# Kernel tuning notes

Hardware: AMD Instinct MI355X
Metric: run time of the kernel (lower is better)

## Reference

```python
import jax, jax.numpy as jnp
import numpy as np

N = 128       # n_channels
B = 131072    # batch
C = np.float32(np.sqrt(0.5))  # 50/50 beamsplitter amplitude (c = s = sqrt(0.5))


def setup_inputs() -> dict:
    key = jax.random.key(0)
    k1, k2, k3, k4 = jax.random.split(key, 4)
    M = N * (N - 1) // 2
    return {
        "x_real": jax.random.normal(k1, (B, N), jnp.float32),
        "x_imag": jax.random.normal(k2, (B, N), jnp.float32),
        "mzi_phases": jax.random.normal(k3, (M * 2,), jnp.float32) * 0.1,
        "output_phases": jax.random.normal(k4, (N,), jnp.float32) * 0.1,
    }


def _construct_unitary(mzi_phases, output_phases):
    n = output_phases.shape[0]
    m = n * (n - 1) // 2
    # pair ordering matches the torch double loop: i ascending, then j > i (row-major triu)
    i_np, j_np = np.triu_indices(n, 1)
    i_idx = jnp.asarray(i_np, jnp.int32)
    j_idx = jnp.asarray(j_np, jnp.int32)
    ph = mzi_phases.reshape(m, 2)
    theta, phi = ph[:, 0], ph[:, 1]

    def step(U, xs):
        th, ph_, i, j = xs
        e_phi = jax.lax.complex(jnp.cos(ph_), jnp.sin(ph_))
        e_th = jax.lax.complex(jnp.cos(th), jnp.sin(th))
        ri = U[i]
        rj = U[j]
        # T_ij @ U touches only rows i and j (O(N) Givens row update)
        new_i = C * ri + (C * e_phi) * rj
        new_j = (C * e_th) * ri - (C * e_th * e_phi) * rj
        U = U.at[i].set(new_i).at[j].set(new_j)
        return U, None

    def chunk_body(U, xs_chunk):
        U, _ = jax.lax.scan(step, U, xs_chunk)
        return U, None

    # chunk the M sequential updates: M = (n-1) * (n//2) for even n;
    # checkpointing chunks keeps reverse-mode memory O(sqrt-ish) instead of O(M * N^2)
    n_chunks = n - 1
    cs = n // 2
    xs = (theta.reshape(n_chunks, cs), phi.reshape(n_chunks, cs),
          i_idx.reshape(n_chunks, cs), j_idx.reshape(n_chunks, cs))
    U0 = jnp.eye(n, dtype=jnp.complex64)
    U, _ = jax.lax.scan(jax.checkpoint(chunk_body), U0, xs)
    # output phase screen D @ U
    d = jax.lax.complex(jnp.cos(output_phases), jnp.sin(output_phases))
    return d[:, None] * U


def reference(x_real, x_imag, mzi_phases, output_phases):
    U = _construct_unitary(mzi_phases, output_phases)           # [N, N] complex64
    x = jax.lax.complex(x_real, x_imag)                          # [B, N] complex64
    # matmul(U, x.unsqueeze(-1)).squeeze(-1) == x @ U^T
    out = jnp.einsum('nm,bm->bn', U, x)                          # [B, N] complex64
    # ComplexDropout is identity in eval mode
    return out
```

## Files before the change

### kernel.cpp

```cpp
#include <hip/hip_runtime.h>
#include <hip/hip_bf16.h>

#define NDIM 128
#define BDIM 131072
#define NMZI 8128
#define NCHUNK 8
#define CSTEP (NMZI / NCHUNK)
#define NJG 8
#define NCOL 32
#define NLOC 16
static constexpr float CC = 0.70710678118654752440f;

typedef __attribute__((ext_vector_type(8))) short bf16x8;
typedef __attribute__((ext_vector_type(4))) float f32x4;

__device__ __align__(16) float2         g_V[NCHUNK * NDIM * NDIM];
__device__ __align__(16) float2         g_W[4 * NDIM * NDIM];
__device__ __align__(16) float2         g_Y[2 * NDIM * NDIM];
__device__ __align__(16) unsigned short g_TB[32 * NDIM * 8];
__device__ __align__(16) unsigned short g_Ur[16 * NDIM * 8];
__device__ __align__(16) unsigned short g_Ui[16 * NDIM * 8];

__device__ inline unsigned short f2bf(float f) {
    union { __hip_bfloat16 h; unsigned short u; } cv;
    cv.h = __float2bfloat16(f);
    return cv.u;
}

__global__ __launch_bounds__(256) void build_scan(const float* __restrict__ mzi) {
    __shared__ float2 Usm[NDIM][NCOL];
    __shared__ float4 phs[CSTEP];
    __shared__ float4 comp[NJG][NCOL];
    const int tid   = threadIdx.x;
    const int c     = tid & 31;
    const int g     = tid >> 5;
    const int col0  = blockIdx.x * NCOL;
    const int chunk = blockIdx.y;
    const int s0 = chunk * CSTEP, s1 = s0 + CSTEP;

    for (int k = g; k < NDIM; k += NJG)
        Usm[k][c] = make_float2((k == col0 + c) ? 1.f : 0.f, 0.f);
    const float2* mzp = (const float2*)mzi;
    for (int t = tid; t < CSTEP; t += 256) {
        const float2 mz = mzp[s0 + t];
        float sp, cp, st, ct;
        sincosf(mz.y, &sp, &cp);
        sincosf(mz.x, &st, &ct);
        phs[t] = make_float4(cp, sp, CC * ct, CC * st);
    }
    __syncthreads();

    int i = 0, base = 0;
    while (base + (NDIM - 1 - i) <= s0) { base += NDIM - 1 - i; ++i; }

    int s = s0;
    while (s < s1) {
        const int cnt  = NDIM - 1 - i;
        const int jA   = i + 1 + (s - base);
        const int L    = min(s1, base + cnt) - s;
        const int nloc = (L + NJG - 1) >> 3;
        const int myBeg = g * nloc;
        const int myN   = max(0, min(nloc, L - myBeg));
        const int pbase = s - s0;

        const float2 r0 = Usm[i][c];

        float2 treg[NLOC];
        float2 qth[NLOC];
        float  A = 1.f;
        float2 Bc = make_float2(0.f, 0.f);
        #pragma unroll
        for (int kk = 0; kk < NLOC; ++kk) {
            if (kk < myN) {
                const int off = myBeg + kk;
                const float4 q  = phs[pbase + off];
                const float2 rj = Usm[jA + off][c];
                const float tr = fmaf(q.x, rj.x, -q.y * rj.y);
                const float ti = fmaf(q.x, rj.y,  q.y * rj.x);
                treg[kk] = make_float2(tr, ti);
                qth[kk]  = make_float2(q.z, q.w);
                Bc.x = CC * (Bc.x + tr);
                Bc.y = CC * (Bc.y + ti);
                A *= CC;
            }
        }
        comp[g][c] = make_float4(A, Bc.x, Bc.y, 0.f);
        __syncthreads();

        float2 r = r0;
        for (int h = 0; h < g; ++h) {
            const float4 cm = comp[h][c];
            r.x = fmaf(cm.x, r.x, cm.y);
            r.y = fmaf(cm.x, r.y, cm.z);
        }

        #pragma unroll
        for (int kk = 0; kk < NLOC; ++kk) {
            if (kk < myN) {
                const float2 t = treg[kk];
                const float2 q = qth[kk];
                const float dr = r.x - t.x, di = r.y - t.y;
                const float njx = fmaf(q.x, dr, -q.y * di);
                const float njy = fmaf(q.x, di,  q.y * dr);
                Usm[jA + myBeg + kk][c] = make_float2(njx, njy);
                r.x = CC * (r.x + t.x);
                r.y = CC * (r.y + t.y);
            }
        }
        if (myN > 0 && (myBeg + myN == L))
            Usm[i][c] = r;
        __syncthreads();

        s += L;
        if (s == base + cnt) { base += cnt; ++i; }
    }

    float2* Vp = g_V + chunk * NDIM * NDIM;
    for (int k = g; k < NDIM; k += NJG)
        Vp[k * NDIM + col0 + c] = Usm[k][c];
}

__global__ __launch_bounds__(128) void compose(int level) {
    const int p = blockIdx.y, n = blockIdx.x, m = threadIdx.x;
    const float2* A; const float2* B; float2* Cout;
    if (level == 0) {
        A = g_V + (2 * p + 1) * NDIM * NDIM;
        B = g_V + (2 * p) * NDIM * NDIM;
        Cout = g_W + p * NDIM * NDIM;
    } else {
        A = g_W + (2 * p + 1) * NDIM * NDIM;
        B = g_W + (2 * p) * NDIM * NDIM;
        Cout = g_Y + p * NDIM * NDIM;
    }
    __shared__ float2 arow[NDIM];
    arow[m] = A[n * NDIM + m];
    __syncthreads();
    float cr = 0.f, ci = 0.f;
    #pragma unroll 8
    for (int k = 0; k < NDIM; ++k) {
        const float2 b = B[k * NDIM + m];
        const float2 a = arow[k];
        cr = fmaf(a.x, b.x, fmaf(-a.y, b.y, cr));
        ci = fmaf(a.x, b.y, fmaf( a.y, b.x, ci));
    }
    Cout[n * NDIM + m] = make_float2(cr, ci);
}

__global__ __launch_bounds__(128) void compose_final(const float* __restrict__ oph) {
    const int n = blockIdx.x, m = threadIdx.x;
    const float2* A = g_Y + NDIM * NDIM;
    const float2* B = g_Y;
    __shared__ float2 arow[NDIM];
    arow[m] = A[n * NDIM + m];
    __syncthreads();
    float cr = 0.f, ci = 0.f;
    #pragma unroll 8
    for (int k = 0; k < NDIM; ++k) {
        const float2 b = B[k * NDIM + m];
        const float2 a = arow[k];
        cr = fmaf(a.x, b.x, fmaf(-a.y, b.y, cr));
        ci = fmaf(a.x, b.y, fmaf( a.y, b.x, ci));
    }
    float ds, dc;
    sincosf(oph[n], &ds, &dc);
    const float vr = fmaf(cr, dc, -ci * ds);
    const float vi = fmaf(cr, ds,  ci * dc);
    const int kg = m >> 3, e = m & 7;
    g_TB[(kg * NDIM + n) * 8 + e]            = f2bf(vr);
    g_TB[((16 + kg) * NDIM + n) * 8 + e]     = f2bf(-vi);
    g_Ur[(kg * NDIM + n) * 8 + e] = f2bf(vr);
    g_Ui[(kg * NDIM + n) * 8 + e] = f2bf(vi);
}

__global__ __launch_bounds__(256, 2) void cmatmul0(const float* __restrict__ xr,
                                                   const float* __restrict__ xi,
                                                   float* __restrict__ out) {
    __shared__ bf16x8 smT[32 * NDIM];
    const int tid  = threadIdx.x;
    const int lane = tid & 63;
    const int w    = tid >> 6;
    const int r15  = lane & 15;
    const int kg4  = lane >> 4;
    const int rbase = blockIdx.x * 256 + w * 16 + r15;

    float4 bufA[16], bufB[16];
    {
        const float* xrp = xr + (size_t)rbase * NDIM;
        const float* xip = xi + (size_t)rbase * NDIM;
        #pragma unroll
        for (int kc = 0; kc < 4; ++kc) {
            const int k0 = kc * 32 + kg4 * 8;
            bufA[kc * 2]     = *(const float4*)(xrp + k0);
            bufA[kc * 2 + 1] = *(const float4*)(xrp + k0 + 4);
            bufA[8 + kc * 2]     = *(const float4*)(xip + k0);
            bufA[8 + kc * 2 + 1] = *(const float4*)(xip + k0 + 4);
        }
    }
    const bf16x8* gT = (const bf16x8*)g_TB;
    for (int t = tid; t < 32 * NDIM; t += 256) smT[t] = gT[t];
    __syncthreads();

    #pragma unroll
    for (int t = 0; t < 4; ++t) {
        float4* cur = (t & 1) ? bufB : bufA;
        float4* nxt = (t & 1) ? bufA : bufB;
        if (t < 3) {
            const int rn = rbase + (t + 1) * 64;
            const float* xrp = xr + (size_t)rn * NDIM;
            const float* xip = xi + (size_t)rn * NDIM;
            #pragma unroll
            for (int kc = 0; kc < 4; ++kc) {
                const int k0 = kc * 32 + kg4 * 8;
                nxt[kc * 2]     = *(const float4*)(xrp + k0);
                nxt[kc * 2 + 1] = *(const float4*)(xrp + k0 + 4);
                nxt[8 + kc * 2]     = *(const float4*)(xip + k0);
                nxt[8 + kc * 2 + 1] = *(const float4*)(xip + k0 + 4);
            }
        }
        bf16x8 fx[8];
        #pragma unroll
        for (int kc2 = 0; kc2 < 8; ++kc2) {
            const float4 lo = cur[kc2 * 2];
            const float4 hi = cur[kc2 * 2 + 1];
            bf16x8 v;
            v[0] = (short)f2bf(lo.x); v[1] = (short)f2bf(lo.y);
            v[2] = (short)f2bf(lo.z); v[3] = (short)f2bf(lo.w);
            v[4] = (short)f2bf(hi.x); v[5] = (short)f2bf(hi.y);
            v[6] = (short)f2bf(hi.z); v[7] = (short)f2bf(hi.w);
            fx[kc2] = v;
        }
        const size_t orow = (size_t)(rbase + t * 64) * NDIM;
        #pragma unroll
        for (int nt = 0; nt < 8; ++nt) {
            f32x4 a0 = {0.f, 0.f, 0.f, 0.f};
            f32x4 a1 = {0.f, 0.f, 0.f, 0.f};
            #pragma unroll
            for (int kc2 = 0; kc2 < 4; ++kc2) {
                const bf16x8 tf = smT[(kc2 * 4 + kg4) * NDIM + nt * 16 + r15];
                a0 = __builtin_amdgcn_mfma_f32_16x16x32_bf16(tf, fx[kc2], a0, 0, 0, 0);
            }
            #pragma unroll
            for (int kc2 = 4; kc2 < 8; ++kc2) {
                const bf16x8 tf = smT[(kc2 * 4 + kg4) * NDIM + nt * 16 + r15];
                a1 = __builtin_amdgcn_mfma_f32_16x16x32_bf16(tf, fx[kc2], a1, 0, 0, 0);
            }
            const f32x4 sum = a0 + a1;
            *(float4*)(out + orow + nt * 16 + kg4 * 4) =
                make_float4(sum[0], sum[1], sum[2], sum[3]);
        }
    }
}

__global__ __launch_bounds__(256) void cmatmul1(const float* __restrict__ xr,
                                                const float* __restrict__ xi,
                                                ushort2* __restrict__ outp) {
    const int lane  = threadIdx.x & 63;
    const int w     = threadIdx.x >> 6;
    const int btile = blockIdx.x * 64 + w * 16;
    const int r15   = lane & 15;
    const int kg4   = lane >> 4;
    const int bload = btile + r15;

    const bf16x8* Ur = (const bf16x8*)g_Ur;
    const bf16x8* Ui = (const bf16x8*)g_Ui;
    const float* xrp = xr + (size_t)bload * NDIM;
    const float* xip = xi + (size_t)bload * NDIM;

    bf16x8 ar[4], ai[4], ain[4];
    #pragma unroll
    for (int kc = 0; kc < 4; ++kc) {
        const int k0 = kc * 32 + kg4 * 8;
        float4 rlo = *(const float4*)(xrp + k0);
        float4 rhi = *(const float4*)(xrp + k0 + 4);
        float4 ilo = *(const float4*)(xip + k0);
        float4 ihi = *(const float4*)(xip + k0 + 4);
        bf16x8 vr, vi, vn;
        vr[0] = (short)f2bf(rlo.x); vr[1] = (short)f2bf(rlo.y);
        vr[2] = (short)f2bf(rlo.z); vr[3] = (short)f2bf(rlo.w);
        vr[4] = (short)f2bf(rhi.x); vr[5] = (short)f2bf(rhi.y);
        vr[6] = (short)f2bf(rhi.z); vr[7] = (short)f2bf(rhi.w);
        vi[0] = (short)f2bf(ilo.x); vi[1] = (short)f2bf(ilo.y);
        vi[2] = (short)f2bf(ilo.z); vi[3] = (short)f2bf(ilo.w);
        vi[4] = (short)f2bf(ihi.x); vi[5] = (short)f2bf(ihi.y);
        vi[6] = (short)f2bf(ihi.z); vi[7] = (short)f2bf(ihi.w);
        #pragma unroll
        for (int e = 0; e < 8; ++e) vn[e] = (short)(vi[e] ^ 0x8000);
        ar[kc] = vr; ai[kc] = vi; ain[kc] = vn;
    }

    #pragma unroll
    for (int nt = 0; nt < 8; ++nt) {
        f32x4 accR = {0.f, 0.f, 0.f, 0.f};
        f32x4 accI = {0.f, 0.f, 0.f, 0.f};
        #pragma unroll
        for (int kc = 0; kc < 4; ++kc) {
            const int kg = kc * 4 + kg4;
            bf16x8 br = Ur[kg * NDIM + nt * 16 + r15];
            bf16x8 bi = Ui[kg * NDIM + nt * 16 + r15];
            accR = __builtin_amdgcn_mfma_f32_16x16x32_bf16(ar[kc],  br, accR, 0, 0, 0);
            accR = __builtin_amdgcn_mfma_f32_16x16x32_bf16(ain[kc], bi, accR, 0, 0, 0);
            accI = __builtin_amdgcn_mfma_f32_16x16x32_bf16(ar[kc],  bi, accI, 0, 0, 0);
            accI = __builtin_amdgcn_mfma_f32_16x16x32_bf16(ai[kc],  br, accI, 0, 0, 0);
        }
        const int n    = nt * 16 + r15;
        const int brow = btile + kg4 * 4;
        #pragma unroll
        for (int r = 0; r < 4; ++r)
            outp[(size_t)(brow + r) * NDIM + n] = make_ushort2(f2bf(accR[r]), f2bf(accI[r]));
    }
}

extern "C" void kernel_launch(void* const* d_in, const int* in_sizes, int n_in,
                              void* d_out, int out_size, void* d_ws, size_t ws_size,
                              hipStream_t stream) {
    const float* xr  = (const float*)d_in[0];
    const float* xi  = (const float*)d_in[1];
    const float* mzi = (const float*)d_in[2];
    const float* oph = (const float*)d_in[3];

    build_scan<<<dim3(4, NCHUNK), dim3(256), 0, stream>>>(mzi);
    compose<<<dim3(NDIM, 4), dim3(128), 0, stream>>>(0);
    compose<<<dim3(NDIM, 2), dim3(128), 0, stream>>>(1);
    compose_final<<<dim3(NDIM), dim3(128), 0, stream>>>(oph);
    if (out_size == BDIM * NDIM) {
        cmatmul0<<<dim3(512), dim3(256), 0, stream>>>(xr, xi, (float*)d_out);
    } else {
        cmatmul1<<<dim3(BDIM / 64), dim3(256), 0, stream>>>(xr, xi, (ushort2*)d_out);
    }
}
```

Baseline: 121.5 us.

## Coalesce x loads via swizzled LDS staging, read U from global, shrink blocks

The matmul kernel now loads each wave's 16 input rows with fully coalesced float4 reads, converts them to bf16 and transposes them through a per-wave XOR-swizzled shared-memory buffer to build the MFMA operands. The U fragments are read straight from global memory (L1/L2 cached) instead of being copied into a 64 KB shared tile. Each block now handles 64 rows with no inner loop, launched as 2048 blocks. The intent is to cut strided-load overhead and LDS occupancy limits, at the cost of losing the explicit load prefetch and repeatedly reading U through the cache.

```diff
diff --git a/kernel.cpp b/kernel.cpp
--- a/kernel.cpp
+++ b/kernel.cpp
@@ -166,88 +166,72 @@
     const float vr = fmaf(cr, dc, -ci * ds);
     const float vi = fmaf(cr, ds,  ci * dc);
     const int kg = m >> 3, e = m & 7;
-    g_TB[(kg * NDIM + n) * 8 + e]            = f2bf(vr);
-    g_TB[((16 + kg) * NDIM + n) * 8 + e]     = f2bf(-vi);
+    g_TB[(kg * NDIM + n) * 8 + e]        = f2bf(vr);
+    g_TB[((16 + kg) * NDIM + n) * 8 + e] = f2bf(-vi);
     g_Ur[(kg * NDIM + n) * 8 + e] = f2bf(vr);
     g_Ui[(kg * NDIM + n) * 8 + e] = f2bf(vi);
 }
 
-__global__ __launch_bounds__(256, 2) void cmatmul0(const float* __restrict__ xr,
-                                                   const float* __restrict__ xi,
-                                                   float* __restrict__ out) {
-    __shared__ bf16x8 smT[32 * NDIM];
+__global__ __launch_bounds__(256) void cmatmul0(const float* __restrict__ xr,
+                                                const float* __restrict__ xi,
+                                                float* __restrict__ out) {
+    __shared__ __align__(16) char smX[4][8192];
     const int tid  = threadIdx.x;
     const int lane = tid & 63;
     const int w    = tid >> 6;
     const int r15  = lane & 15;
     const int kg4  = lane >> 4;
-    const int rbase = blockIdx.x * 256 + w * 16 + r15;
-
-    float4 bufA[16], bufB[16];
-    {
-        const float* xrp = xr + (size_t)rbase * NDIM;
-        const float* xip = xi + (size_t)rbase * NDIM;
-        #pragma unroll
-        for (int kc = 0; kc < 4; ++kc) {
-            const int k0 = kc * 32 + kg4 * 8;
-            bufA[kc * 2]     = *(const float4*)(xrp + k0);
-            bufA[kc * 2 + 1] = *(const float4*)(xrp + k0 + 4);
-            bufA[8 + kc * 2]     = *(const float4*)(xip + k0);
-            bufA[8 + kc * 2 + 1] = *(const float4*)(xip + k0 + 4);
-        }
-    }
+    const int l31  = lane & 31;
+    const int lh   = lane >> 5;
+    const int R    = blockIdx.x * 64 + w * 16;
+
+    const float4* sre = (const float4*)(xr + (size_t)R * NDIM);
+    const float4* sim = (const float4*)(xi + (size_t)R * NDIM);
+    float4 G[16];
+    #pragma unroll
+    for (int p = 0; p < 8; ++p) G[p]     = sre[p * 64 + lane];
+    #pragma unroll
+    for (int p = 0; p < 8; ++p) G[8 + p] = sim[p * 64 + lane];
+
+    char* buf = &smX[w][0];
+    #pragma unroll
+    for (int p = 0; p < 8; ++p) {
+        const int row = 2 * p + lh;
+        const int swz = (row & 7) << 4;
+        uint2 v;
+        v.x = ((unsigned)f2bf(G[p].y) << 16) | f2bf(G[p].x);
+        v.y = ((unsigned)f2bf(G[p].w) << 16) | f2bf(G[p].z);
+        *(uint2*)(buf + row * 512 + ((l31 * 8) ^ swz)) = v;
+        v.x = ((unsigned)f2bf(G[8 + p].y) << 16) | f2bf(G[8 + p].x);
+        v.y = ((unsigned)f2bf(G[8 + p].w) << 16) | f2bf(G[8 + p].z);
+        *(uint2*)(buf + row * 512 + 256 + ((l31 * 8) ^ swz)) = v;
+    }
+
+    bf16x8 fx[8];
+    const int rswz = (r15 & 7) << 4;
+    #pragma unroll
+    for (int kc = 0; kc < 8; ++kc) {
+        const int off = (((kc & 3) * 64 + kg4 * 16) ^ rswz) + ((kc >= 4) ? 256 : 0);
+        fx[kc] = *(const bf16x8*)(buf + r15 * 512 + off);
+    }
+
     const bf16x8* gT = (const bf16x8*)g_TB;
-    for (int t = tid; t < 32 * NDIM; t += 256) smT[t] = gT[t];
-    __syncthreads();
-
-    #pragma unroll
-    for (int t = 0; t < 4; ++t) {
-        float4* cur = (t & 1) ? bufB : bufA;
-        float4* nxt = (t & 1) ? bufA : bufB;
-        if (t < 3) {
-            const int rn = rbase + (t + 1) * 64;
-            const float* xrp = xr + (size_t)rn * NDIM;
-            const float* xip = xi + (size_t)rn * NDIM;
-            #pragma unroll
-            for (int kc = 0; kc < 4; ++kc) {
-                const int k0 = kc * 32 + kg4 * 8;
-                nxt[kc * 2]     = *(const float4*)(xrp + k0);
-                nxt[kc * 2 + 1] = *(const float4*)(xrp + k0 + 4);
-                nxt[8 + kc * 2]     = *(const float4*)(xip + k0);
-                nxt[8 + kc * 2 + 1] = *(const float4*)(xip + k0 + 4);
-            }
-        }
-        bf16x8 fx[8];
-        #pragma unroll
-        for (int kc2 = 0; kc2 < 8; ++kc2) {
-            const float4 lo = cur[kc2 * 2];
-            const float4 hi = cur[kc2 * 2 + 1];
-            bf16x8 v;
-            v[0] = (short)f2bf(lo.x); v[1] = (short)f2bf(lo.y);
-            v[2] = (short)f2bf(lo.z); v[3] = (short)f2bf(lo.w);
-            v[4] = (short)f2bf(hi.x); v[5] = (short)f2bf(hi.y);
-            v[6] = (short)f2bf(hi.z); v[7] = (short)f2bf(hi.w);
-            fx[kc2] = v;
-        }
-        const size_t orow = (size_t)(rbase + t * 64) * NDIM;
-        #pragma unroll
-        for (int nt = 0; nt < 8; ++nt) {
-            f32x4 a0 = {0.f, 0.f, 0.f, 0.f};
-            f32x4 a1 = {0.f, 0.f, 0.f, 0.f};
-            #pragma unroll
-            for (int kc2 = 0; kc2 < 4; ++kc2) {
-                const bf16x8 tf = smT[(kc2 * 4 + kg4) * NDIM + nt * 16 + r15];
-                a0 = __builtin_amdgcn_mfma_f32_16x16x32_bf16(tf, fx[kc2], a0, 0, 0, 0);
-            }
-            #pragma unroll
-            for (int kc2 = 4; kc2 < 8; ++kc2) {
-                const bf16x8 tf = smT[(kc2 * 4 + kg4) * NDIM + nt * 16 + r15];
-                a1 = __builtin_amdgcn_mfma_f32_16x16x32_bf16(tf, fx[kc2], a1, 0, 0, 0);
-            }
-            const f32x4 sum = a0 + a1;
-            *(float4*)(out + orow + nt * 16 + kg4 * 4) =
-                make_float4(sum[0], sum[1], sum[2], sum[3]);
-        }
+    const size_t orow = (size_t)(R + r15) * NDIM;
+    #pragma unroll
+    for (int nt = 0; nt < 8; ++nt) {
+        f32x4 a0 = {0.f, 0.f, 0.f, 0.f};
+        f32x4 a1 = {0.f, 0.f, 0.f, 0.f};
+        #pragma unroll
+        for (int kc = 0; kc < 4; ++kc)
+            a0 = __builtin_amdgcn_mfma_f32_16x16x32_bf16(
+                gT[(kc * 4 + kg4) * NDIM + nt * 16 + r15], fx[kc], a0, 0, 0, 0);
+        #pragma unroll
+        for (int kc = 4; kc < 8; ++kc)
+            a1 = __builtin_amdgcn_mfma_f32_16x16x32_bf16(
+                gT[(kc * 4 + kg4) * NDIM + nt * 16 + r15], fx[kc], a1, 0, 0, 0);
+        const f32x4 s = a0 + a1;
+        *(float4*)(out + orow + nt * 16 + kg4 * 4) =
+            make_float4(s[0], s[1], s[2], s[3]);
     }
 }
 
@@ -323,7 +307,7 @@
     compose<<<dim3(NDIM, 2), dim3(128), 0, stream>>>(1);
     compose_final<<<dim3(NDIM), dim3(128), 0, stream>>>(oph);
     if (out_size == BDIM * NDIM) {
-        cmatmul0<<<dim3(512), dim3(256), 0, stream>>>(xr, xi, (float*)d_out);
+        cmatmul0<<<dim3(BDIM / 64), dim3(256), 0, stream>>>(xr, xi, (float*)d_out);
     } else {
         cmatmul1<<<dim3(BDIM / 64), dim3(256), 0, stream>>>(xr, xi, (ushort2*)d_out);
     }
```

Result: no change. 122.7 us (+1.0%).
